# Optimization experiments

Measured on AMD Instinct MI355X. Metric: run time of the kernel, lower is better.

The kernel has to match this reference:

```python
import jax, jax.numpy as jnp
import numpy as np

NUM_HEADS = 16
ROPE_BASE = 10000.0

def rotate_half(x):
    h = x.shape[-1] // 2
    return jnp.concatenate([-x[..., h:], x[..., :h]], axis=-1)

def rope_cos_sin(seq_len, head_dim, dtype):
    inv_freq = 1.0 / (ROPE_BASE ** (jnp.arange(0, head_dim, 2, dtype=jnp.float32) / head_dim))
    t = jnp.arange(seq_len, dtype=jnp.float32)
    freqs = jnp.outer(t, inv_freq)              # [N, hd/2]
    emb = jnp.concatenate([freqs, freqs], -1)   # [N, hd]
    return jnp.cos(emb).astype(dtype), jnp.sin(emb).astype(dtype)

def setup_inputs() -> dict:
    key = jax.random.key(0)
    ks = jax.random.split(key, 5)
    B, N, D = 2, 2048, 1024
    s = 1.0 / np.sqrt(D)
    return {
        "x": jax.random.normal(ks[0], (B, N, D), jnp.float32),
        "attention_mask": jnp.ones((B, N), jnp.int32),
        "Wq": jax.random.normal(ks[1], (D, D), jnp.float32) * s,
        "Wk": jax.random.normal(ks[2], (D, D), jnp.float32) * s,
        "Wv": jax.random.normal(ks[3], (D, D), jnp.float32) * s,
        "Wo": jax.random.normal(ks[4], (D, D), jnp.float32) * s,
    }

def reference(x, attention_mask, Wq, Wk, Wv, Wo):
    B, N, D = x.shape
    H = NUM_HEADS
    hd = D // H
    scale = hd ** -0.5
    # projections (nn.Linear: x @ W.T), split heads -> [B, H, N, hd]
    q = jnp.einsum('bnd,ed->bne', x, Wq).reshape(B, N, H, hd).transpose(0, 2, 1, 3)
    k = jnp.einsum('bnd,ed->bne', x, Wk).reshape(B, N, H, hd).transpose(0, 2, 1, 3)
    v = jnp.einsum('bnd,ed->bne', x, Wv).reshape(B, N, H, hd).transpose(0, 2, 1, 3)
    cos, sin = rope_cos_sin(N, hd, x.dtype)     # [N, hd]
    cos = cos[None, None]; sin = sin[None, None]
    q = q * cos + rotate_half(q) * sin
    k = k * cos + rotate_half(k) * sin
    attn = jnp.einsum('bhqd,bhkd->bhqk', q, k) * scale
    mask = attention_mask.astype(bool)[:, None, None, :]        # [B,1,1,N]
    attn = jnp.where(mask, attn, -jnp.inf)
    all_masked = (attention_mask.sum(-1) == 0)[:, None, None, None]
    attn = jnp.where(all_masked, 0.0, attn)
    attn = jax.nn.softmax(attn, axis=-1)
    out = jnp.einsum('bhqk,bhkd->bhqd', attn, v)
    out = out.transpose(0, 2, 1, 3).reshape(B, N, D)
    return jnp.einsum('bnd,ed->bne', out, Wo)
```

## Files before the change

### kernel.cpp

```cpp
#include <hip/hip_runtime.h>
#include <math.h>

#define BATCH 2
#define SEQ   2048
#define DM    1024
#define NH    16
#define HD    64
#define MTOT  (BATCH*SEQ)

typedef short v8s __attribute__((ext_vector_type(8)));
typedef short v4s __attribute__((ext_vector_type(4)));
typedef float v4f __attribute__((ext_vector_type(4)));

#define MFMA16(a, b, c) __builtin_amdgcn_mfma_f32_16x16x32_bf16((a), (b), (c), 0, 0, 0)

__device__ __forceinline__ short f2b(float f) {
    union { float f; unsigned u; } v; v.f = f;
    return (short)((v.u + 0x8000u) >> 16);
}

__device__ __forceinline__ float fexp2(float x) {
    float r; asm("v_exp_f32 %0, %1" : "=v"(r) : "v"(x)); return r;
}

__device__ __forceinline__ void gload16(const void* g, void* lds) {
    __builtin_amdgcn_global_load_lds(
        (const __attribute__((address_space(1))) void*)g,
        (__attribute__((address_space(3))) void*)lds, 16, 0, 0);
}

__device__ __forceinline__ void rope_cs(int n, float f_rev, float* c, float* s) {
    float rev = (float)n * f_rev;
    float t = rev - floorf(rev);
    float ang = t * 6.283185307179586f;
    *c = __cosf(ang);
    *s = __sinf(ang);
}

#define L2_1E4_D32 0.4152410118609203f
#define INV2PI     0.15915494309189535f
#define QSCALE     0.18033688011112042f

__global__ __launch_bounds__(256) void cvt_all_kernel(
    const float* __restrict__ x,  const float* __restrict__ wq,
    const float* __restrict__ wk, const float* __restrict__ wv,
    const float* __restrict__ wo, short* __restrict__ dst)
{
    int i = blockIdx.x * 256 + threadIdx.x;
    const float* src; int off;
    if (i < (1 << 19)) { src = x; off = i; }
    else {
        int j = i - (1 << 19);
        int wsel = j >> 17;
        off = j & ((1 << 17) - 1);
        src = (wsel == 0) ? wq : (wsel == 1) ? wk : (wsel == 2) ? wv : wo;
    }
    const float4* s4 = (const float4*)src;
    float4 a = s4[2 * off], b = s4[2 * off + 1];
    v8s p;
    p[0] = f2b(a.x); p[1] = f2b(a.y); p[2] = f2b(a.z); p[3] = f2b(a.w);
    p[4] = f2b(b.x); p[5] = f2b(b.y); p[6] = f2b(b.z); p[7] = f2b(b.w);
    *(v8s*)&dst[8 * i] = p;
}

__global__ __launch_bounds__(256, 3) void qkv_rope_mfma(
    const short* __restrict__ xb, const short* __restrict__ Wqb,
    const short* __restrict__ Wkb, const short* __restrict__ Wvb,
    short* __restrict__ K, short* __restrict__ Vt, short* __restrict__ Qb)
{
    const int zz = blockIdx.z;
    const short* __restrict__ Wb = (zz == 0) ? Wkb : (zz == 1) ? Wvb : Wqb;
    const int m0 = blockIdx.x * 128, e00 = blockIdx.y * 128;
    const int tid = threadIdx.x;
    const int w = tid >> 6, lane = tid & 63, lq = lane >> 4, lr = lane & 15;
    const int wm = w >> 1, wn = w & 1;

    __shared__ union {
        struct { short As[2][128][32]; short Bs[2][128][32]; } p1;
        short Css[128][136];
    } u;

    v4f acc[4][4];
    #pragma unroll
    for (int i = 0; i < 4; ++i)
        for (int j = 0; j < 4; ++j)
            for (int r = 0; r < 4; ++r) acc[i][j][r] = 0.f;

    const int gr = lane >> 2, gc = 8 * (lane & 3);
    for (int k0 = 0; k0 < DM; k0 += 64) {
        __syncthreads();
        #pragma unroll
        for (int ks = 0; ks < 2; ++ks) {
            gload16(&xb[(size_t)(m0 + 32 * w      + gr) * DM + k0 + 32 * ks + gc],
                    &u.p1.As[ks][32 * w][0]);
            gload16(&xb[(size_t)(m0 + 32 * w + 16 + gr) * DM + k0 + 32 * ks + gc],
                    &u.p1.As[ks][32 * w + 16][0]);
            gload16(&Wb[(size_t)(e00 + 32 * w      + gr) * DM + k0 + 32 * ks + gc],
                    &u.p1.Bs[ks][32 * w][0]);
            gload16(&Wb[(size_t)(e00 + 32 * w + 16 + gr) * DM + k0 + 32 * ks + gc],
                    &u.p1.Bs[ks][32 * w + 16][0]);
        }
        __syncthreads();
        #pragma unroll
        for (int ks = 0; ks < 2; ++ks) {
            v8s af[4], bf[4];
            #pragma unroll
            for (int i = 0; i < 4; ++i)
                af[i] = *(const v8s*)&u.p1.As[ks][64 * wm + 16 * i + lr][8 * lq];
            #pragma unroll
            for (int j = 0; j < 4; ++j)
                bf[j] = *(const v8s*)&u.p1.Bs[ks][64 * wn + 16 * j + lr][8 * lq];
            #pragma unroll
            for (int i = 0; i < 4; ++i)
                #pragma unroll
                for (int j = 0; j < 4; ++j)
                    acc[i][j] = MFMA16(af[i], bf[j], acc[i][j]);
        }
    }
    __syncthreads();

    const int b = m0 >> 11, n00 = m0 & (SEQ - 1);

    if (zz != 1) {
        short* __restrict__ dst = (zz == 0) ? K : Qb;
        const float sc = (zz == 0) ? 1.0f : QSCALE;
        float f0 = exp2f(-(float)lr * L2_1E4_D32) * INV2PI;
        float f1 = exp2f(-(float)(16 + lr) * L2_1E4_D32) * INV2PI;
        #pragma unroll
        for (int i = 0; i < 4; ++i) {
            #pragma unroll
            for (int r = 0; r < 4; ++r) {
                int row = 64 * wm + 16 * i + 4 * lq + r;
                int n = n00 + row;
                float c0v, s0v, c1v, s1v;
                rope_cs(n, f0, &c0v, &s0v);
                rope_cs(n, f1, &c1v, &s1v);
                float q0 = acc[i][0][r], q1 = acc[i][1][r];
                float q2 = acc[i][2][r], q3 = acc[i][3][r];
                u.Css[row][64 * wn + lr]      = f2b(sc * (q0 * c0v - q2 * s0v));
                u.Css[row][64 * wn + 16 + lr] = f2b(sc * (q1 * c1v - q3 * s1v));
                u.Css[row][64 * wn + 32 + lr] = f2b(sc * (q2 * c0v + q0 * s0v));
                u.Css[row][64 * wn + 48 + lr] = f2b(sc * (q3 * c1v + q1 * s1v));
            }
        }
        __syncthreads();
        int row = tid >> 1, hh = tid & 1;
        int h = (e00 >> 6) + hh;
        int n = n00 + row;
        size_t base = (((size_t)(b * NH + h)) * SEQ + n) * HD;
        #pragma unroll
        for (int p = 0; p < 8; ++p)
            *(v8s*)&dst[base + 8 * p] = *(const v8s*)&u.Css[row][64 * hh + 8 * p];
    } else {
        #pragma unroll
        for (int i = 0; i < 4; ++i) {
            #pragma unroll
            for (int j = 0; j < 4; ++j) {
                v4s t;
                #pragma unroll
                for (int r = 0; r < 4; ++r) t[r] = f2b(acc[i][j][r]);
                *(v4s*)&u.Css[64 * wn + 16 * j + lr][64 * wm + 16 * i + 4 * lq] = t;
            }
        }
        __syncthreads();
        int c = tid >> 1, half = (tid & 1) * 64;
        int h = (e00 + c) >> 6, d = (e00 + c) & 63;
        size_t base = (((size_t)(b * NH + h)) * HD + d) * SEQ + n00 + half;
        #pragma unroll
        for (int p = 0; p < 8; ++p)
            *(v8s*)&Vt[base + 8 * p] = *(const v8s*)&u.Css[c][half + 8 * p];
    }
}

#define SWZ(tile, row, bo) ((char*)&(tile)[row][0] + ((bo) ^ (((row) & 7) << 4)))

__global__ __launch_bounds__(512, 4) void attn_mfma(
    const short* __restrict__ Qb, const short* __restrict__ K,
    const short* __restrict__ Vt, const int* __restrict__ mask,
    short* __restrict__ O)
{
    const int flat = blockIdx.y * 32 + blockIdx.x;
    const int lg   = (flat & 7) * 64 + (flat >> 3);
    const int m0 = (lg & 31) * 128, h = lg >> 5;
    const int b = m0 >> 11, n0 = m0 & (SEQ - 1), bh = b * NH + h;
    const int tid = threadIdx.x;
    const int w = tid >> 6, lane = tid & 63, lq = lane >> 4, lr = lane & 15;

    __shared__ short Ks[128][64];
    __shared__ short Vs[64][128];
    __shared__ short Ps[128][64];
    __shared__ float mbias[128];

    const short* __restrict__ Qh = Qb + (size_t)bh * SEQ * HD;
    v8s aq[2];
    #pragma unroll
    for (int ks = 0; ks < 2; ++ks)
        aq[ks] = *(const v8s*)&Qh[(size_t)(n0 + 16 * w + lr) * HD + 32 * ks + 8 * lq];

    float lacc[4] = {0.f, 0.f, 0.f, 0.f};
    v4f o[4];
    #pragma unroll
    for (int nt = 0; nt < 4; ++nt)
        for (int r = 0; r < 4; ++r) o[nt][r] = 0.f;

    const int kr = tid >> 2, kc = (tid & 3) * 16;
    const int kb = 32 * (tid & 3);
    const int krh = kr & 63;
    const int pkr = 64 * (kr >> 6) + 16 * (krh & 3) + (krh >> 2);
    const int vr = tid >> 3, vc = (tid & 7) * 16;
    const int vb = 32 * (tid & 7);
    const short* __restrict__ Kb = K + (size_t)bh * SEQ * HD;
    const short* __restrict__ Vb = Vt + (size_t)bh * HD * SEQ;

    v8s k1 = *(const v8s*)&Kb[(size_t)kr * HD + kc];
    v8s k2 = *(const v8s*)&Kb[(size_t)kr * HD + kc + 8];
    v8s v1 = *(const v8s*)&Vb[(size_t)vr * SEQ + vc];
    v8s v2 = *(const v8s*)&Vb[(size_t)vr * SEQ + vc + 8];
    int mnext = ((tid & 3) == 0) ? mask[b * SEQ + kr] : 0;

    for (int c0 = 0; c0 < SEQ; c0 += 128) {
        __syncthreads();
        *(v8s*)SWZ(Ks, pkr, kb)      = k1;
        *(v8s*)SWZ(Ks, pkr, kb + 16) = k2;
        *(v8s*)SWZ(Vs, vr, vb)       = v1;
        *(v8s*)SWZ(Vs, vr, vb + 16)  = v2;
        if ((tid & 3) == 0) mbias[pkr] = mnext ? -24.0f : -1e30f;
        __syncthreads();
        if (c0 + 128 < SEQ) {
            k1 = *(const v8s*)&Kb[(size_t)(c0 + 128 + kr) * HD + kc];
            k2 = *(const v8s*)&Kb[(size_t)(c0 + 128 + kr) * HD + kc + 8];
            v1 = *(const v8s*)&Vb[(size_t)vr * SEQ + c0 + 128 + vc];
            v2 = *(const v8s*)&Vb[(size_t)vr * SEQ + c0 + 128 + vc + 8];
            if ((tid & 3) == 0) mnext = mask[b * SEQ + c0 + 128 + kr];
        }

        #pragma unroll
        for (int half = 0; half < 2; ++half) {
            v8s kf[2][4];
            #pragma unroll
            for (int ks = 0; ks < 2; ++ks)
                #pragma unroll
                for (int nt = 0; nt < 4; ++nt)
                    kf[ks][nt] = *(const v8s*)SWZ(Ks, 64 * half + 16 * nt + lr,
                                                  64 * ks + 16 * lq);
            float bias[4];
            #pragma unroll
            for (int nt = 0; nt < 4; ++nt)
                bias[nt] = mbias[64 * half + 16 * nt + lr];

            v4f sv[4];
            #pragma unroll
            for (int nt = 0; nt < 4; ++nt)
                for (int r = 0; r < 4; ++r) sv[nt][r] = 0.f;
            #pragma unroll
            for (int ks = 0; ks < 2; ++ks)
                #pragma unroll
                for (int nt = 0; nt < 4; ++nt)
                    sv[nt] = MFMA16(aq[ks], kf[ks][nt], sv[nt]);

            #pragma unroll
            for (int r = 0; r < 4; ++r) {
                float p0 = fexp2(sv[0][r] + bias[0]);
                float p1 = fexp2(sv[1][r] + bias[1]);
                float p2 = fexp2(sv[2][r] + bias[2]);
                float p3 = fexp2(sv[3][r] + bias[3]);
                lacc[r] += (p0 + p1) + (p2 + p3);
                unsigned u0, u1;
                asm("v_cvt_pk_bf16_f32 %0, %1, %2" : "=v"(u0) : "v"(p0), "v"(p1));
                asm("v_cvt_pk_bf16_f32 %0, %1, %2" : "=v"(u1) : "v"(p2), "v"(p3));
                uint2 pk; pk.x = u0; pk.y = u1;
                int prow = 16 * w + 4 * lq + r;
                *(uint2*)SWZ(Ps, prow, 8 * lr) = pk;
            }
            #pragma unroll
            for (int ks = 0; ks < 2; ++ks) {
                v8s a = *(const v8s*)SWZ(Ps, 16 * w + lr, 64 * ks + 16 * lq);
                #pragma unroll
                for (int nt = 0; nt < 4; ++nt) {
                    v8s vf = *(const v8s*)SWZ(Vs, 16 * nt + lr,
                                              128 * half + 64 * ks + 16 * lq);
                    o[nt] = MFMA16(a, vf, o[nt]);
                }
            }
        }
    }

    #pragma unroll
    for (int r = 0; r < 4; ++r) {
        float l = lacc[r];
        l += __shfl_xor(l, 1);
        l += __shfl_xor(l, 2);
        l += __shfl_xor(l, 4);
        l += __shfl_xor(l, 8);
        float inv = (l > 0.f) ? 1.f / l : 0.f;
        int qrow = 16 * w + 4 * lq + r;
        #pragma unroll
        for (int nt = 0; nt < 4; ++nt)
            O[(size_t)(m0 + qrow) * DM + h * HD + 16 * nt + lr] =
                f2b(o[nt][r] * inv);
    }
}

__global__ __launch_bounds__(256, 2) void oproj_mfma(
    const short* __restrict__ O, const short* __restrict__ Wob,
    float* __restrict__ out)
{
    const int m0 = blockIdx.x * 64, e00 = blockIdx.y * 128;
    const int tid = threadIdx.x;
    const int w = tid >> 6, lane = tid & 63, lq = lane >> 4, lr = lane & 15;

    __shared__ short As[2][64][32];
    __shared__ short Bs[2][128][32];

    v4f acc[4][2];
    #pragma unroll
    for (int i = 0; i < 4; ++i)
        for (int j = 0; j < 2; ++j)
            for (int r = 0; r < 4; ++r) acc[i][j][r] = 0.f;

    const int gr = lane >> 2, gc = 8 * (lane & 3);
    for (int k0 = 0; k0 < DM; k0 += 64) {
        __syncthreads();
        #pragma unroll
        for (int ks = 0; ks < 2; ++ks) {
            gload16(&O[(size_t)(m0 + 16 * w + gr) * DM + k0 + 32 * ks + gc],
                    &As[ks][16 * w][0]);
            gload16(&Wob[(size_t)(e00 + 32 * w      + gr) * DM + k0 + 32 * ks + gc],
                    &Bs[ks][32 * w][0]);
            gload16(&Wob[(size_t)(e00 + 32 * w + 16 + gr) * DM + k0 + 32 * ks + gc],
                    &Bs[ks][32 * w + 16][0]);
        }
        __syncthreads();
        #pragma unroll
        for (int ks = 0; ks < 2; ++ks) {
            v8s af[4], bf[2];
            #pragma unroll
            for (int i = 0; i < 4; ++i)
                af[i] = *(const v8s*)&As[ks][16 * i + lr][8 * lq];
            #pragma unroll
            for (int j = 0; j < 2; ++j)
                bf[j] = *(const v8s*)&Bs[ks][32 * w + 16 * j + lr][8 * lq];
            #pragma unroll
            for (int i = 0; i < 4; ++i)
                #pragma unroll
                for (int j = 0; j < 2; ++j)
                    acc[i][j] = MFMA16(af[i], bf[j], acc[i][j]);
        }
    }

    #pragma unroll
    for (int i = 0; i < 4; ++i)
        #pragma unroll
        for (int r = 0; r < 4; ++r) {
            int m = m0 + 16 * i + 4 * lq + r;
            #pragma unroll
            for (int j = 0; j < 2; ++j)
                out[(size_t)m * DM + e00 + 32 * w + 16 * j + lr] = acc[i][j][r];
        }
}

extern "C" void kernel_launch(void* const* d_in, const int* in_sizes, int n_in,
                              void* d_out, int out_size, void* d_ws, size_t ws_size,
                              hipStream_t stream)
{
    const float* x    = (const float*)d_in[0];
    const int*   mask = (const int*)d_in[1];
    const float* Wq   = (const float*)d_in[2];
    const float* Wk   = (const float*)d_in[3];
    const float* Wv   = (const float*)d_in[4];
    const float* Wo   = (const float*)d_in[5];
    float* out = (float*)d_out;

    short* xb  = (short*)d_ws;
    short* Wqb = xb  + (size_t)MTOT * DM;
    short* Wkb = Wqb + (size_t)DM * DM;
    short* Wvb = Wkb + (size_t)DM * DM;
    short* Wob = Wvb + (size_t)DM * DM;
    short* Qb  = Wob + (size_t)DM * DM;
    short* O   = xb;
    short* K  = (short*)d_out;
    short* Vt = K + (size_t)MTOT * DM;

    cvt_all_kernel<<<4096, 256, 0, stream>>>(x, Wq, Wk, Wv, Wo, xb);

    dim3 g1(MTOT / 128, DM / 128, 3);
    qkv_rope_mfma<<<g1, 256, 0, stream>>>(xb, Wqb, Wkb, Wvb, K, Vt, Qb);

    dim3 g2(MTOT / 128, NH);
    attn_mfma<<<g2, 512, 0, stream>>>(Qb, K, Vt, mask, O);

    dim3 g3(MTOT / 64, DM / 128);
    oproj_mfma<<<g3, 256, 0, stream>>>(O, Wob, out);
}
```

Measured before the change: 190.4 us.

## Rewrite attention kernel with 32x32 MFMA tiles and 4-wave blocks

The attention kernel moves from 16x16x32 to 32x32x16 bf16 MFMA. Each of 4 waves now owns 32 query rows instead of 16 rows across 8 waves, and S is computed as K·Q so each lane's probabilities map directly into a small per-wave P buffer. A wave-uniform fast path skips the per-column mask bias lookup when the whole key tile is unmasked. The row-sum normalisation goes through shared memory for the transposed output layout. Larger tiles reduce LDS fragment traffic per MFMA, but halving the wave count per block lowers parallelism and raises register pressure.

```diff
diff --git a/kernel.cpp b/kernel.cpp
--- a/kernel.cpp
+++ b/kernel.cpp
@@ -11,8 +11,10 @@
 typedef short v8s __attribute__((ext_vector_type(8)));
 typedef short v4s __attribute__((ext_vector_type(4)));
 typedef float v4f __attribute__((ext_vector_type(4)));
+typedef float v16f __attribute__((ext_vector_type(16)));
 
 #define MFMA16(a, b, c) __builtin_amdgcn_mfma_f32_16x16x32_bf16((a), (b), (c), 0, 0, 0)
+#define MFMA32(a, b, c) __builtin_amdgcn_mfma_f32_32x32x16_bf16((a), (b), (c), 0, 0, 0)
 
 __device__ __forceinline__ short f2b(float f) {
     union { float f; unsigned u; } v; v.f = f;
@@ -174,7 +176,7 @@
 
 #define SWZ(tile, row, bo) ((char*)&(tile)[row][0] + ((bo) ^ (((row) & 7) << 4)))
 
-__global__ __launch_bounds__(512, 4) void attn_mfma(
+__global__ __launch_bounds__(256, 2) void attn_mfma(
     const short* __restrict__ Qb, const short* __restrict__ K,
     const short* __restrict__ Vt, const int* __restrict__ mask,
     short* __restrict__ O)
@@ -184,120 +186,125 @@
     const int m0 = (lg & 31) * 128, h = lg >> 5;
     const int b = m0 >> 11, n0 = m0 & (SEQ - 1), bh = b * NH + h;
     const int tid = threadIdx.x;
-    const int w = tid >> 6, lane = tid & 63, lq = lane >> 4, lr = lane & 15;
+    const int w = tid >> 6, lane = tid & 63;
+    const int l31 = lane & 31, hi = lane >> 5;
 
     __shared__ short Ks[128][64];
     __shared__ short Vs[64][128];
-    __shared__ short Ps[128][64];
+    __shared__ short Ps[4][32][40];
     __shared__ float mbias[128];
+    __shared__ float linv[128];
 
     const short* __restrict__ Qh = Qb + (size_t)bh * SEQ * HD;
-    v8s aq[2];
-    #pragma unroll
-    for (int ks = 0; ks < 2; ++ks)
-        aq[ks] = *(const v8s*)&Qh[(size_t)(n0 + 16 * w + lr) * HD + 32 * ks + 8 * lq];
-
-    float lacc[4] = {0.f, 0.f, 0.f, 0.f};
-    v4f o[4];
-    #pragma unroll
-    for (int nt = 0; nt < 4; ++nt)
-        for (int r = 0; r < 4; ++r) o[nt][r] = 0.f;
-
-    const int kr = tid >> 2, kc = (tid & 3) * 16;
-    const int kb = 32 * (tid & 3);
-    const int krh = kr & 63;
-    const int pkr = 64 * (kr >> 6) + 16 * (krh & 3) + (krh >> 2);
-    const int vr = tid >> 3, vc = (tid & 7) * 16;
-    const int vb = 32 * (tid & 7);
+    v8s qf[4];
+    #pragma unroll
+    for (int ds = 0; ds < 4; ++ds)
+        qf[ds] = *(const v8s*)&Qh[(size_t)(n0 + 32 * w + l31) * HD + 16 * ds + 8 * hi];
+
+    v16f o0, o1;
+    #pragma unroll
+    for (int r = 0; r < 16; ++r) { o0[r] = 0.f; o1[r] = 0.f; }
+    float lacc = 0.f;
+
+    const int kr2 = tid >> 1, kc2 = (tid & 1) * 32;
+    const int vr2 = tid >> 2, vc2 = (tid & 3) * 32;
     const short* __restrict__ Kb = K + (size_t)bh * SEQ * HD;
     const short* __restrict__ Vb = Vt + (size_t)bh * HD * SEQ;
 
-    v8s k1 = *(const v8s*)&Kb[(size_t)kr * HD + kc];
-    v8s k2 = *(const v8s*)&Kb[(size_t)kr * HD + kc + 8];
-    v8s v1 = *(const v8s*)&Vb[(size_t)vr * SEQ + vc];
-    v8s v2 = *(const v8s*)&Vb[(size_t)vr * SEQ + vc + 8];
-    int mnext = ((tid & 3) == 0) ? mask[b * SEQ + kr] : 0;
+    v8s kpre[4], vpre[4];
+    #pragma unroll
+    for (int j = 0; j < 4; ++j) {
+        kpre[j] = *(const v8s*)&Kb[(size_t)kr2 * HD + kc2 + 8 * j];
+        vpre[j] = *(const v8s*)&Vb[(size_t)vr2 * SEQ + vc2 + 8 * j];
+    }
+    int mnext = (tid < 128) ? mask[b * SEQ + tid] : 0;
 
     for (int c0 = 0; c0 < SEQ; c0 += 128) {
         __syncthreads();
-        *(v8s*)SWZ(Ks, pkr, kb)      = k1;
-        *(v8s*)SWZ(Ks, pkr, kb + 16) = k2;
-        *(v8s*)SWZ(Vs, vr, vb)       = v1;
-        *(v8s*)SWZ(Vs, vr, vb + 16)  = v2;
-        if ((tid & 3) == 0) mbias[pkr] = mnext ? -24.0f : -1e30f;
+        #pragma unroll
+        for (int j = 0; j < 4; ++j) {
+            *(v8s*)SWZ(Ks, kr2, 2 * kc2 + 16 * j) = kpre[j];
+            *(v8s*)SWZ(Vs, vr2, 2 * vc2 + 16 * j) = vpre[j];
+        }
+        if (tid < 128) mbias[tid] = mnext ? -24.0f : -1e30f;
         __syncthreads();
         if (c0 + 128 < SEQ) {
-            k1 = *(const v8s*)&Kb[(size_t)(c0 + 128 + kr) * HD + kc];
-            k2 = *(const v8s*)&Kb[(size_t)(c0 + 128 + kr) * HD + kc + 8];
-            v1 = *(const v8s*)&Vb[(size_t)vr * SEQ + c0 + 128 + vc];
-            v2 = *(const v8s*)&Vb[(size_t)vr * SEQ + c0 + 128 + vc + 8];
-            if ((tid & 3) == 0) mnext = mask[b * SEQ + c0 + 128 + kr];
-        }
-
-        #pragma unroll
-        for (int half = 0; half < 2; ++half) {
-            v8s kf[2][4];
-            #pragma unroll
-            for (int ks = 0; ks < 2; ++ks)
+            #pragma unroll
+            for (int j = 0; j < 4; ++j) {
+                kpre[j] = *(const v8s*)&Kb[(size_t)(c0 + 128 + kr2) * HD + kc2 + 8 * j];
+                vpre[j] = *(const v8s*)&Vb[(size_t)vr2 * SEQ + c0 + 128 + vc2 + 8 * j];
+            }
+            if (tid < 128) mnext = mask[b * SEQ + c0 + 128 + tid];
+        }
+
+        float mb0 = mbias[lane], mb1 = mbias[64 + lane];
+        int allv = __all(mb0 > -1e29f && mb1 > -1e29f);
+
+        #pragma unroll
+        for (int kt = 0; kt < 4; ++kt) {
+            v8s kf[4];
+            #pragma unroll
+            for (int ds = 0; ds < 4; ++ds)
+                kf[ds] = *(const v8s*)SWZ(Ks, 32 * kt + l31, 32 * ds + 16 * hi);
+
+            v16f s;
+            #pragma unroll
+            for (int r = 0; r < 16; ++r) s[r] = 0.f;
+            #pragma unroll
+            for (int ds = 0; ds < 4; ++ds)
+                s = MFMA32(kf[ds], qf[ds], s);
+
+            if (allv) {
                 #pragma unroll
-                for (int nt = 0; nt < 4; ++nt)
-                    kf[ks][nt] = *(const v8s*)SWZ(Ks, 64 * half + 16 * nt + lr,
-                                                  64 * ks + 16 * lq);
-            float bias[4];
-            #pragma unroll
-            for (int nt = 0; nt < 4; ++nt)
-                bias[nt] = mbias[64 * half + 16 * nt + lr];
-
-            v4f sv[4];
-            #pragma unroll
-            for (int nt = 0; nt < 4; ++nt)
-                for (int r = 0; r < 4; ++r) sv[nt][r] = 0.f;
-            #pragma unroll
-            for (int ks = 0; ks < 2; ++ks)
+                for (int g = 0; g < 4; ++g) {
+                    float p0 = fexp2(s[4 * g + 0] - 24.0f);
+                    float p1 = fexp2(s[4 * g + 1] - 24.0f);
+                    float p2 = fexp2(s[4 * g + 2] - 24.0f);
+                    float p3 = fexp2(s[4 * g + 3] - 24.0f);
+                    lacc += (p0 + p1) + (p2 + p3);
+                    unsigned u0, u1;
+                    asm("v_cvt_pk_bf16_f32 %0, %1, %2" : "=v"(u0) : "v"(p0), "v"(p1));
+                    asm("v_cvt_pk_bf16_f32 %0, %1, %2" : "=v"(u1) : "v"(p2), "v"(p3));
+                    uint2 pk; pk.x = u0; pk.y = u1;
+                    *(uint2*)&Ps[w][l31][8 * g + 4 * hi] = pk;
+                }
+            } else {
                 #pragma unroll
-                for (int nt = 0; nt < 4; ++nt)
-                    sv[nt] = MFMA16(aq[ks], kf[ks][nt], sv[nt]);
-
-            #pragma unroll
-            for (int r = 0; r < 4; ++r) {
-                float p0 = fexp2(sv[0][r] + bias[0]);
-                float p1 = fexp2(sv[1][r] + bias[1]);
-                float p2 = fexp2(sv[2][r] + bias[2]);
-                float p3 = fexp2(sv[3][r] + bias[3]);
-                lacc[r] += (p0 + p1) + (p2 + p3);
-                unsigned u0, u1;
-                asm("v_cvt_pk_bf16_f32 %0, %1, %2" : "=v"(u0) : "v"(p0), "v"(p1));
-                asm("v_cvt_pk_bf16_f32 %0, %1, %2" : "=v"(u1) : "v"(p2), "v"(p3));
-                uint2 pk; pk.x = u0; pk.y = u1;
-                int prow = 16 * w + 4 * lq + r;
-                *(uint2*)SWZ(Ps, prow, 8 * lr) = pk;
-            }
-            #pragma unroll
-            for (int ks = 0; ks < 2; ++ks) {
-                v8s a = *(const v8s*)SWZ(Ps, 16 * w + lr, 64 * ks + 16 * lq);
-                #pragma unroll
-                for (int nt = 0; nt < 4; ++nt) {
-                    v8s vf = *(const v8s*)SWZ(Vs, 16 * nt + lr,
-                                              128 * half + 64 * ks + 16 * lq);
-                    o[nt] = MFMA16(a, vf, o[nt]);
+                for (int g = 0; g < 4; ++g) {
+                    float p0 = fexp2(s[4 * g + 0] + mbias[32 * kt + 8 * g + 4 * hi + 0]);
+                    float p1 = fexp2(s[4 * g + 1] + mbias[32 * kt + 8 * g + 4 * hi + 1]);
+                    float p2 = fexp2(s[4 * g + 2] + mbias[32 * kt + 8 * g + 4 * hi + 2]);
+                    float p3 = fexp2(s[4 * g + 3] + mbias[32 * kt + 8 * g + 4 * hi + 3]);
+                    lacc += (p0 + p1) + (p2 + p3);
+                    unsigned u0, u1;
+                    asm("v_cvt_pk_bf16_f32 %0, %1, %2" : "=v"(u0) : "v"(p0), "v"(p1));
+                    asm("v_cvt_pk_bf16_f32 %0, %1, %2" : "=v"(u1) : "v"(p2), "v"(p3));
+                    uint2 pk; pk.x = u0; pk.y = u1;
+                    *(uint2*)&Ps[w][l31][8 * g + 4 * hi] = pk;
                 }
             }
-        }
-    }
-
-    #pragma unroll
-    for (int r = 0; r < 4; ++r) {
-        float l = lacc[r];
-        l += __shfl_xor(l, 1);
-        l += __shfl_xor(l, 2);
-        l += __shfl_xor(l, 4);
-        l += __shfl_xor(l, 8);
-        float inv = (l > 0.f) ? 1.f / l : 0.f;
-        int qrow = 16 * w + 4 * lq + r;
-        #pragma unroll
-        for (int nt = 0; nt < 4; ++nt)
-            O[(size_t)(m0 + qrow) * DM + h * HD + 16 * nt + lr] =
-                f2b(o[nt][r] * inv);
+
+            #pragma unroll
+            for (int ks = 0; ks < 2; ++ks) {
+                v8s pa = *(const v8s*)&Ps[w][l31][16 * ks + 8 * hi];
+                v8s vf0 = *(const v8s*)SWZ(Vs, l31,      64 * kt + 32 * ks + 16 * hi);
+                v8s vf1 = *(const v8s*)SWZ(Vs, l31 + 32, 64 * kt + 32 * ks + 16 * hi);
+                o0 = MFMA32(pa, vf0, o0);
+                o1 = MFMA32(pa, vf1, o1);
+            }
+        }
+    }
+
+    lacc += __shfl_xor(lacc, 32);
+    float inv = (lacc > 0.f) ? 1.f / lacc : 0.f;
+    if (lane < 32) linv[32 * w + l31] = inv;
+    #pragma unroll
+    for (int r = 0; r < 16; ++r) {
+        const int q = (r & 3) + 8 * (r >> 2);
+        float iv = linv[32 * w + q + 4 * hi];
+        size_t base = (size_t)(m0 + 32 * w + q + 4 * hi) * DM + h * HD + l31;
+        O[base]      = f2b(o0[r] * iv);
+        O[base + 32] = f2b(o1[r] * iv);
     }
 }
 
@@ -387,7 +394,7 @@
     qkv_rope_mfma<<<g1, 256, 0, stream>>>(xb, Wqb, Wkb, Wvb, K, Vt, Qb);
 
     dim3 g2(MTOT / 128, NH);
-    attn_mfma<<<g2, 512, 0, stream>>>(Qb, K, Vt, mask, O);
+    attn_mfma<<<g2, 256, 0, stream>>>(Qb, K, Vt, mask, O);
 
     dim3 g3(MTOT / 64, DM / 128);
     oproj_mfma<<<g3, 256, 0, stream>>>(O, Wob, out);
```

Measured after the change: 188.5 us. Within noise of the previous version (-1.0%).
